# Optimization experiments

Measured on AMD Instinct MI355X. Metric: run time of the kernel, lower is better.

Reference implementation:

```python
import jax, jax.numpy as jnp
import numpy as np

N_NODES = 100000
N_EDGES = 1600000


def setup_inputs() -> dict:
    key = jax.random.key(0)
    k1, k2, k3, k4, k5, k6 = jax.random.split(key, 6)
    x = jax.random.normal(k1, (N_NODES, 2), dtype=jnp.float32)
    edge_index = jax.random.randint(k2, (2, N_EDGES), 0, N_NODES, dtype=jnp.int64)
    # Glorot-style init for GCN weights, zeros for biases (PyG defaults)
    W1 = jax.random.normal(k3, (2, 64), dtype=jnp.float32) * (1.0 / np.sqrt(2.0))
    b1 = jnp.zeros((64,), dtype=jnp.float32)
    W2 = jax.random.normal(k4, (64, 1), dtype=jnp.float32) * (1.0 / np.sqrt(64.0))
    b2 = jnp.zeros((1,), dtype=jnp.float32)
    return {"x": x, "edge_index": edge_index, "W1": W1, "b1": b1, "W2": W2, "b2": b2}


def reference(x, edge_index, W1, b1, W2, b2):
    N = x.shape[0]
    row, col = edge_index[0], edge_index[1]  # source, target (PyG flow source_to_target)
    # symmetric GCN normalization, degrees from target index (no self loops)
    deg = jax.ops.segment_sum(jnp.ones(edge_index.shape[1], x.dtype), col, num_segments=N)
    deg_inv_sqrt = jnp.where(deg > 0, jnp.where(deg > 0, deg, 1.0) ** -0.5, 0.0)
    norm = (deg_inv_sqrt[row] * deg_inv_sqrt[col])[:, None]  # [E,1]

    def gcn_conv(h, W, b):
        h = h @ W                       # [N,F_out] tiny GEMM
        msg = h[row] * norm             # gather + scale: [E,F_out]
        agg = jax.ops.segment_sum(msg, col, num_segments=N)  # scatter-add
        return agg + b

    h = jax.nn.relu(gcn_conv(x, W1, b1))   # dropout is identity in eval mode
    out = jax.nn.relu(gcn_conv(h, W2, b2))
    return out
```

## Files before the change

### kernel.cpp

```cpp
#include <hip/hip_runtime.h>
#include <math.h>

#define NN 100000
#define NE 1600000
#define BSHIFT 8
#define BKT 256
#define NB 391
#define NBP 392
#define EPB 4096
#define NPB 391
#define STRIDE 5120
#define RT 512

__global__ void __launch_bounds__(RT) reorder_kernel(
        const int* __restrict__ row, const int* __restrict__ col,
        int* __restrict__ cursor, unsigned* __restrict__ packed) {
    __shared__ int h[NBP], lb[NBP], gb[NBP];
    __shared__ int wsum[RT / 64];
    __shared__ unsigned st[EPB];
    __shared__ unsigned short sbkt[EPB];
    const int t = threadIdx.x;
    const int lane = t & 63, wid = t >> 6;
    const int e0 = blockIdx.x * EPB;
    const int n = min(EPB, NE - e0);

    for (int i = t; i < NBP; i += RT) h[i] = 0;
    __syncthreads();

    const int4* rv = (const int4*)(row + e0);
    const int4* cv = (const int4*)(col + e0);
    unsigned pk[8]; int bb[8];
#pragma unroll
    for (int u = 0; u < 8; ++u) bb[u] = -1;
#pragma unroll
    for (int g = 0; g < 2; ++g) {
        int grp = g * RT + t;
        if (4 * grp < n) {
            int4 r4 = rv[grp], c4 = cv[grp];
            int rr[4] = {r4.x, r4.y, r4.z, r4.w};
            int cc[4] = {c4.x, c4.y, c4.z, c4.w};
#pragma unroll
            for (int j = 0; j < 4; ++j) {
                pk[4 * g + j] = ((unsigned)rr[j] << BSHIFT) | (unsigned)(cc[j] & (BKT - 1));
                bb[4 * g + j] = cc[j] >> BSHIFT;
            }
        }
    }
#pragma unroll
    for (int u = 0; u < 8; ++u)
        if (bb[u] >= 0) atomicAdd(&h[bb[u]], 1);
    __syncthreads();

    int v = (t < NBP) ? h[t] : 0;
    int incl = v;
#pragma unroll
    for (int d = 1; d < 64; d <<= 1) {
        int u = __shfl_up(incl, d);
        if (lane >= d) incl += u;
    }
    if (lane == 63) wsum[wid] = incl;
    __syncthreads();
    int off = 0;
#pragma unroll
    for (int j = 0; j < RT / 64 - 1; ++j)
        if (j < wid) off += wsum[j];
    if (t < NB) {
        lb[t] = off + incl - v;
        gb[t] = v ? atomicAdd(&cursor[t], v) : 0;
    }
    __syncthreads();
    for (int i = t; i < NBP; i += RT) h[i] = 0;
    __syncthreads();

#pragma unroll
    for (int u = 0; u < 8; ++u) {
        if (bb[u] >= 0) {
            int r = atomicAdd(&h[bb[u]], 1);
            int idx = lb[bb[u]] + r;
            st[idx] = pk[u];
            sbkt[idx] = (unsigned short)bb[u];
        }
    }
    __syncthreads();
    for (int i = t; i < n; i += RT) {
        int b = sbkt[i];
        int pos = gb[b] + (i - lb[b]);
        if (pos < STRIDE)
            packed[b * STRIDE + pos] = st[i];
    }
}

__global__ void __launch_bounds__(RT) sortb_kernel(
        const unsigned* __restrict__ packed, const int* __restrict__ cursor,
        const float2* __restrict__ x2,
        unsigned* __restrict__ srow, int2* __restrict__ node_rng,
        float* __restrict__ dis, float2* __restrict__ y2) {
    __shared__ int cnt[BKT], rk[BKT], sexA[BKT];
    __shared__ int wsum[RT / 64];
    __shared__ unsigned st[STRIDE];
    __shared__ unsigned srt[STRIDE];
    const int t = threadIdx.x;
    const int lane = t & 63, wid = t >> 6;
    const int b = blockIdx.x;
    const int s0 = b * STRIDE;
    const int L = min(cursor[b], STRIDE);

    if (t < BKT) { cnt[t] = 0; rk[t] = 0; }
    __syncthreads();
    for (int i = t; i < L; i += RT) {
        unsigned p = packed[s0 + i];
        st[i] = p;
        atomicAdd(&cnt[p & (BKT - 1u)], 1);
    }
    __syncthreads();

    int v = (t < BKT) ? cnt[t] : 0;
    int incl = v;
#pragma unroll
    for (int d = 1; d < 64; d <<= 1) {
        int u = __shfl_up(incl, d);
        if (lane >= d) incl += u;
    }
    if (lane == 63 && wid < BKT / 64) wsum[wid] = incl;
    __syncthreads();
    int off = 0;
#pragma unroll
    for (int j = 0; j < BKT / 64 - 1; ++j)
        if (j < wid) off += wsum[j];
    if (t < BKT) {
        int sex = off + incl - v;
        sexA[t] = sex;
        int node = (b << BSHIFT) + t;
        if (node < NN) {
            float dv = (v > 0) ? rsqrtf((float)v) : 0.0f;
            dis[node] = dv;
            float2 xv = x2[node];
            y2[node] = make_float2(xv.x * dv, xv.y * dv);
            node_rng[node] = make_int2(s0 + sex, s0 + sex + v);
        }
    }
    __syncthreads();

    for (int i = t; i < L; i += RT) {
        unsigned p = st[i];
        int cl = p & (BKT - 1u);
        int r = atomicAdd(&rk[cl], 1);
        srt[sexA[cl] + r] = p >> BSHIFT;
    }
    __syncthreads();
    for (int i = t; i < L; i += RT) srow[s0 + i] = srt[i];
}

__global__ void conv1_kernel(const unsigned* __restrict__ srow, const int2* __restrict__ node_rng,
                             const float2* __restrict__ y2, const float* __restrict__ dis,
                             const float* __restrict__ W1, const float* __restrict__ b1,
                             const float* __restrict__ W2, float* __restrict__ z2) {
    __shared__ float sW0[64], sW1[64], sb1[64], sW2[64];
    int t = threadIdx.x;
    if (t < 64) { sW0[t] = W1[t]; sW1[t] = W1[64 + t]; sb1[t] = b1[t]; sW2[t] = W2[t]; }
    __syncthreads();
    int lane = t & 3;
    int node = blockIdx.x * 64 + (t >> 2);
    if (node >= NN) return;
    int2 rng = node_rng[node];
    float sx = 0.f, sy = 0.f;
    for (int k = rng.x + lane; k < rng.y; k += 4) {
        float2 v = y2[srow[k]];
        sx += v.x; sy += v.y;
    }
    sx += __shfl_xor(sx, 1); sy += __shfl_xor(sy, 1);
    sx += __shfl_xor(sx, 2); sy += __shfl_xor(sy, 2);
    float dv = dis[node];
    float a0 = sx * dv, a1 = sy * dv;
    float acc = 0.0f;
    int j0 = lane * 16;
#pragma unroll
    for (int jj = 0; jj < 16; ++jj) {
        int j = j0 + jj;
        float h = fmaf(a0, sW0[j], fmaf(a1, sW1[j], sb1[j]));
        acc = fmaf(fmaxf(h, 0.0f), sW2[j], acc);
    }
    acc += __shfl_xor(acc, 1);
    acc += __shfl_xor(acc, 2);
    if (lane == 0) z2[node] = acc * dv;
}

__global__ void conv2_kernel(const unsigned* __restrict__ srow, const int2* __restrict__ node_rng,
                             const float* __restrict__ z2, const float* __restrict__ dis,
                             const float* __restrict__ b2, float* __restrict__ out) {
    int t = threadIdx.x;
    int lane = t & 3;
    int node = blockIdx.x * 64 + (t >> 2);
    if (node >= NN) return;
    int2 rng = node_rng[node];
    float s = 0.f;
    for (int k = rng.x + lane; k < rng.y; k += 4)
        s += z2[srow[k]];
    s += __shfl_xor(s, 1);
    s += __shfl_xor(s, 2);
    if (lane == 0)
        out[node] = fmaxf(fmaf(dis[node], s, b2[0]), 0.0f);
}

extern "C" void kernel_launch(void* const* d_in, const int* in_sizes, int n_in,
                              void* d_out, int out_size, void* d_ws, size_t ws_size,
                              hipStream_t stream) {
    const float* x  = (const float*)d_in[0];
    const int*   ei = (const int*)d_in[1];
    const float* W1 = (const float*)d_in[2];
    const float* b1 = (const float*)d_in[3];
    const float* W2 = (const float*)d_in[4];
    const float* b2 = (const float*)d_in[5];
    float* out = (float*)d_out;

    const int* row = ei;
    const int* col = ei + NE;

    unsigned* packed   = (unsigned*)d_ws;
    unsigned* srow     = packed + (size_t)NB * STRIDE;
    float2*   y2       = (float2*)(srow + (size_t)NB * STRIDE);
    float*    dis      = (float*)(y2 + NN);
    float*    z2       = dis + NN;
    int2*     node_rng = (int2*)(z2 + NN);
    int*      cursor   = (int*)(node_rng + NN);

    hipMemsetAsync(cursor, 0, NB * sizeof(int), stream);

    reorder_kernel<<<NPB, RT, 0, stream>>>(row, col, cursor, packed);
    sortb_kernel  <<<NB, RT, 0, stream>>>(packed, cursor, (const float2*)x,
                                          srow, node_rng, dis, y2);
    conv1_kernel  <<<(NN + 63) / 64, 256, 0, stream>>>(srow, node_rng, y2, dis,
                                                       W1, b1, W2, z2);
    conv2_kernel  <<<(NN + 63) / 64, 256, 0, stream>>>(srow, node_rng, z2, dis, b2, out);
}
```

Measured before the change: 119.4 us.

## Replace per-bucket sort with shared-memory atomic aggregation per destination bucket

Drops the second-level sort that built a CSR (srow plus node ranges). Degree, conv1 and conv2 now each scan the bucketed packed edge list and accumulate per destination node with shared-memory float atomics inside a 1024-thread block per 256-node bucket. This removes the sort pass and the node_rng/srow traffic. In exchange the packed list is read three times, there is LDS atomic contention on high-degree nodes, and the float summation order becomes nondeterministic. Only 391 blocks are launched per kernel, which may underfill the GPU.

After: 129.8 us. 8.7% more time.

```diff
diff --git a/kernel.cpp b/kernel.cpp
--- a/kernel.cpp
+++ b/kernel.cpp
@@ -11,10 +11,11 @@
 #define NPB 391
 #define STRIDE 5120
 #define RT 512
+#define CT 1024
 
 __global__ void __launch_bounds__(RT) reorder_kernel(
         const int* __restrict__ row, const int* __restrict__ col,
-        int* __restrict__ cursor, unsigned* __restrict__ packed) {
+        unsigned* __restrict__ cursor, unsigned* __restrict__ packed) {
     __shared__ int h[NBP], lb[NBP], gb[NBP];
     __shared__ int wsum[RT / 64];
     __shared__ unsigned st[EPB];
@@ -66,7 +67,7 @@
         if (j < wid) off += wsum[j];
     if (t < NB) {
         lb[t] = off + incl - v;
-        gb[t] = v ? atomicAdd(&cursor[t], v) : 0;
+        gb[t] = v ? (int)atomicAdd(&cursor[t], (unsigned)v) : 0;
     }
     __syncthreads();
     for (int i = t; i < NBP; i += RT) h[i] = 0;
@@ -90,116 +91,93 @@
     }
 }
 
-__global__ void __launch_bounds__(RT) sortb_kernel(
-        const unsigned* __restrict__ packed, const int* __restrict__ cursor,
-        const float2* __restrict__ x2,
-        unsigned* __restrict__ srow, int2* __restrict__ node_rng,
-        float* __restrict__ dis, float2* __restrict__ y2) {
-    __shared__ int cnt[BKT], rk[BKT], sexA[BKT];
-    __shared__ int wsum[RT / 64];
-    __shared__ unsigned st[STRIDE];
-    __shared__ unsigned srt[STRIDE];
-    const int t = threadIdx.x;
-    const int lane = t & 63, wid = t >> 6;
+__global__ void __launch_bounds__(CT) deg_kernel(
+        const unsigned* __restrict__ packed, const unsigned* __restrict__ cursor,
+        const float2* __restrict__ x2, float* __restrict__ dis, float2* __restrict__ y2) {
+    __shared__ int cnt[BKT];
+    const int t = threadIdx.x;
     const int b = blockIdx.x;
+    if (t < BKT) cnt[t] = 0;
+    __syncthreads();
     const int s0 = b * STRIDE;
-    const int L = min(cursor[b], STRIDE);
-
-    if (t < BKT) { cnt[t] = 0; rk[t] = 0; }
-    __syncthreads();
-    for (int i = t; i < L; i += RT) {
+    const int L = min((int)cursor[b], STRIDE);
+    for (int i = t; i < L; i += CT)
+        atomicAdd(&cnt[packed[s0 + i] & (BKT - 1u)], 1);
+    __syncthreads();
+    int node = (b << BSHIFT) + t;
+    if (t < BKT && node < NN) {
+        int v = cnt[t];
+        float dv = (v > 0) ? rsqrtf((float)v) : 0.0f;
+        dis[node] = dv;
+        float2 xv = x2[node];
+        y2[node] = make_float2(xv.x * dv, xv.y * dv);
+    }
+}
+
+__global__ void __launch_bounds__(CT) conv1_kernel(
+        const unsigned* __restrict__ packed, const unsigned* __restrict__ cursor,
+        const float2* __restrict__ y2, const float* __restrict__ dis,
+        const float* __restrict__ W1, const float* __restrict__ b1,
+        const float* __restrict__ W2, float* __restrict__ z2) {
+    __shared__ float ax[BKT], ay[BKT];
+    __shared__ float sW0[64], sW1[64], sb1[64], sW2[64];
+    const int t = threadIdx.x;
+    const int b = blockIdx.x;
+    if (t < BKT) { ax[t] = 0.0f; ay[t] = 0.0f; }
+    else if (t < BKT + 64) {
+        int j = t - BKT;
+        sW0[j] = W1[j]; sW1[j] = W1[64 + j]; sb1[j] = b1[j]; sW2[j] = W2[j];
+    }
+    __syncthreads();
+    const int s0 = b * STRIDE;
+    const int L = min((int)cursor[b], STRIDE);
+    for (int i = t; i < L; i += CT) {
         unsigned p = packed[s0 + i];
-        st[i] = p;
-        atomicAdd(&cnt[p & (BKT - 1u)], 1);
-    }
-    __syncthreads();
-
-    int v = (t < BKT) ? cnt[t] : 0;
-    int incl = v;
-#pragma unroll
-    for (int d = 1; d < 64; d <<= 1) {
-        int u = __shfl_up(incl, d);
-        if (lane >= d) incl += u;
-    }
-    if (lane == 63 && wid < BKT / 64) wsum[wid] = incl;
-    __syncthreads();
-    int off = 0;
-#pragma unroll
-    for (int j = 0; j < BKT / 64 - 1; ++j)
-        if (j < wid) off += wsum[j];
-    if (t < BKT) {
-        int sex = off + incl - v;
-        sexA[t] = sex;
-        int node = (b << BSHIFT) + t;
-        if (node < NN) {
-            float dv = (v > 0) ? rsqrtf((float)v) : 0.0f;
-            dis[node] = dv;
-            float2 xv = x2[node];
-            y2[node] = make_float2(xv.x * dv, xv.y * dv);
-            node_rng[node] = make_int2(s0 + sex, s0 + sex + v);
+        float2 v = y2[p >> BSHIFT];
+        int cl = p & (BKT - 1u);
+        atomicAdd(&ax[cl], v.x);
+        atomicAdd(&ay[cl], v.y);
+    }
+    __syncthreads();
+    const int lane = t & 3;
+    const int nl = t >> 2;
+    const int node = (b << BSHIFT) + nl;
+    if (node < NN) {
+        float dv = dis[node];
+        float a0 = ax[nl] * dv, a1 = ay[nl] * dv;
+        float acc = 0.0f;
+        const int j0 = lane * 16;
+#pragma unroll
+        for (int jj = 0; jj < 16; ++jj) {
+            int j = j0 + jj;
+            float h = fmaf(a0, sW0[j], fmaf(a1, sW1[j], sb1[j]));
+            acc = fmaf(fmaxf(h, 0.0f), sW2[j], acc);
         }
-    }
-    __syncthreads();
-
-    for (int i = t; i < L; i += RT) {
-        unsigned p = st[i];
-        int cl = p & (BKT - 1u);
-        int r = atomicAdd(&rk[cl], 1);
-        srt[sexA[cl] + r] = p >> BSHIFT;
-    }
-    __syncthreads();
-    for (int i = t; i < L; i += RT) srow[s0 + i] = srt[i];
-}
-
-__global__ void conv1_kernel(const unsigned* __restrict__ srow, const int2* __restrict__ node_rng,
-                             const float2* __restrict__ y2, const float* __restrict__ dis,
-                             const float* __restrict__ W1, const float* __restrict__ b1,
-                             const float* __restrict__ W2, float* __restrict__ z2) {
-    __shared__ float sW0[64], sW1[64], sb1[64], sW2[64];
-    int t = threadIdx.x;
-    if (t < 64) { sW0[t] = W1[t]; sW1[t] = W1[64 + t]; sb1[t] = b1[t]; sW2[t] = W2[t]; }
-    __syncthreads();
-    int lane = t & 3;
-    int node = blockIdx.x * 64 + (t >> 2);
-    if (node >= NN) return;
-    int2 rng = node_rng[node];
-    float sx = 0.f, sy = 0.f;
-    for (int k = rng.x + lane; k < rng.y; k += 4) {
-        float2 v = y2[srow[k]];
-        sx += v.x; sy += v.y;
-    }
-    sx += __shfl_xor(sx, 1); sy += __shfl_xor(sy, 1);
-    sx += __shfl_xor(sx, 2); sy += __shfl_xor(sy, 2);
-    float dv = dis[node];
-    float a0 = sx * dv, a1 = sy * dv;
-    float acc = 0.0f;
-    int j0 = lane * 16;
-#pragma unroll
-    for (int jj = 0; jj < 16; ++jj) {
-        int j = j0 + jj;
-        float h = fmaf(a0, sW0[j], fmaf(a1, sW1[j], sb1[j]));
-        acc = fmaf(fmaxf(h, 0.0f), sW2[j], acc);
-    }
-    acc += __shfl_xor(acc, 1);
-    acc += __shfl_xor(acc, 2);
-    if (lane == 0) z2[node] = acc * dv;
-}
-
-__global__ void conv2_kernel(const unsigned* __restrict__ srow, const int2* __restrict__ node_rng,
-                             const float* __restrict__ z2, const float* __restrict__ dis,
-                             const float* __restrict__ b2, float* __restrict__ out) {
-    int t = threadIdx.x;
-    int lane = t & 3;
-    int node = blockIdx.x * 64 + (t >> 2);
-    if (node >= NN) return;
-    int2 rng = node_rng[node];
-    float s = 0.f;
-    for (int k = rng.x + lane; k < rng.y; k += 4)
-        s += z2[srow[k]];
-    s += __shfl_xor(s, 1);
-    s += __shfl_xor(s, 2);
-    if (lane == 0)
-        out[node] = fmaxf(fmaf(dis[node], s, b2[0]), 0.0f);
+        acc += __shfl_xor(acc, 1);
+        acc += __shfl_xor(acc, 2);
+        if (lane == 0) z2[node] = acc * dv;
+    }
+}
+
+__global__ void __launch_bounds__(CT) conv2_kernel(
+        const unsigned* __restrict__ packed, const unsigned* __restrict__ cursor,
+        const float* __restrict__ z2, const float* __restrict__ dis,
+        const float* __restrict__ b2, float* __restrict__ out) {
+    __shared__ float acc[BKT];
+    const int t = threadIdx.x;
+    const int b = blockIdx.x;
+    if (t < BKT) acc[t] = 0.0f;
+    __syncthreads();
+    const int s0 = b * STRIDE;
+    const int L = min((int)cursor[b], STRIDE);
+    for (int i = t; i < L; i += CT) {
+        unsigned p = packed[s0 + i];
+        atomicAdd(&acc[p & (BKT - 1u)], z2[p >> BSHIFT]);
+    }
+    __syncthreads();
+    int node = (b << BSHIFT) + t;
+    if (t < BKT && node < NN)
+        out[node] = fmaxf(fmaf(dis[node], acc[t], b2[0]), 0.0f);
 }
 
 extern "C" void kernel_launch(void* const* d_in, const int* in_sizes, int n_in,
@@ -216,20 +194,16 @@
     const int* row = ei;
     const int* col = ei + NE;
 
-    unsigned* packed   = (unsigned*)d_ws;
-    unsigned* srow     = packed + (size_t)NB * STRIDE;
-    float2*   y2       = (float2*)(srow + (size_t)NB * STRIDE);
-    float*    dis      = (float*)(y2 + NN);
-    float*    z2       = dis + NN;
-    int2*     node_rng = (int2*)(z2 + NN);
-    int*      cursor   = (int*)(node_rng + NN);
-
-    hipMemsetAsync(cursor, 0, NB * sizeof(int), stream);
+    unsigned* packed = (unsigned*)d_ws;
+    float2*   y2     = (float2*)(packed + (size_t)NB * STRIDE);
+    float*    dis    = (float*)(y2 + NN);
+    float*    z2     = dis + NN;
+    unsigned* cursor = (unsigned*)(z2 + NN);
+
+    hipMemsetAsync(cursor, 0, NB * sizeof(unsigned), stream);
 
     reorder_kernel<<<NPB, RT, 0, stream>>>(row, col, cursor, packed);
-    sortb_kernel  <<<NB, RT, 0, stream>>>(packed, cursor, (const float2*)x,
-                                          srow, node_rng, dis, y2);
-    conv1_kernel  <<<(NN + 63) / 64, 256, 0, stream>>>(srow, node_rng, y2, dis,
-                                                       W1, b1, W2, z2);
-    conv2_kernel  <<<(NN + 63) / 64, 256, 0, stream>>>(srow, node_rng, z2, dis, b2, out);
-}
+    deg_kernel    <<<NB, CT, 0, stream>>>(packed, cursor, (const float2*)x, dis, y2);
+    conv1_kernel  <<<NB, CT, 0, stream>>>(packed, cursor, y2, dis, W1, b1, W2, z2);
+    conv2_kernel  <<<NB, CT, 0, stream>>>(packed, cursor, z2, dis, b2, out);
+}
```
